# Kernel optimization log

Measured on AMD Instinct MI355X. Metric: run time of the kernel, lower is better.

## Reference

```python
import jax, jax.numpy as jnp
import numpy as np

BS, TLEN, NNODE, DIM = 32, 6, 4, 1500
HID = 128; D2 = 2 * HID
LSTMH, LSTMO, KCONV = 64, 128, 3
CONV_OUT = 191
DECAY = 0.7
WIN, STRIDES = (2, 2), (1, 2)
FEAT_IN = LSTMO * CONV_OUT  # 24448


def _bn(x, p, axis):
    # eval-mode BatchNorm: p = [gamma, beta, running_mean, running_var] stacked [4, C]
    sh = [1] * x.ndim; sh[axis] = -1
    g, b, m, v = (p[i].reshape(sh) for i in range(4))
    return (x - m) * (g * jax.lax.rsqrt(v + 1e-5)) + b


def _conv1d(x, w, pad):  # x [B,C,L], w [O,I,K]
    return jax.lax.conv_general_dilated(x, w, (1,), [(pad, pad)],
                                        dimension_numbers=('NCH', 'OIH', 'NCH'))


def _maxpool2(x):  # MaxPool1d(kernel=2, stride=2, padding=1) with -inf padding
    x = jnp.pad(x, ((0, 0), (0, 0), (1, 1)), constant_values=-jnp.inf)
    return jax.lax.reduce_window(x, -jnp.inf, jax.lax.max, (1, 1, 2), (1, 1, 2), 'VALID')


def _mpnn_block(x, w, s, gw, gb, bnA, tw, tb, bnM):
    # x: [bs, tlen, ns, d]; Conv_GraphST windowing + dot-graph + masked adj + 1-hop MPNN + mean pool
    bs, tlen, ns, d = x.shape
    nw = (tlen - w) // s + 1
    con = jnp.stack([x[:, j * s:j * s + w] for j in range(nw)], axis=1)  # [bs,nw,w,ns,d]
    Xc = con.reshape(bs * nw, w * ns, d)  # node index = t*ns + sensor (time-major)
    f = Xc @ gw + gb
    N = w * ns
    eye = jnp.eye(N, dtype=x.dtype)
    Adj = jnp.einsum('bnd,bmd->bnm', f, f)
    Adj = jax.nn.softmax(jax.nn.leaky_relu(Adj - eye * 1e8), axis=-1) + eye
    t = jnp.arange(N) // ns
    mask = DECAY ** jnp.abs(t[:, None] - t[None, :]).astype(x.dtype)  # Mask_Matrix decay
    Adj = Adj * mask
    Xb = _bn(Xc, bnA, -1)  # BN over feature channel (transpose-BN-transpose in torch)
    h = jnp.einsum('bnm,bmd->bnd', Adj, Xb) @ tw + tb
    h = jax.nn.leaky_relu(_bn(h, bnM, -1))
    return h.reshape(bs, nw, w, ns, -1).mean(axis=2)  # mean pool over window-time


def _pos_encoding(tlen, d):
    pos = jnp.arange(tlen, dtype=jnp.float32)[:, None]
    div = jnp.exp(jnp.arange(0, d, 2, dtype=jnp.float32) * (-np.log(100.0) / d))
    pe = jnp.zeros((tlen, d), jnp.float32)
    return pe.at[:, 0::2].set(jnp.sin(pos * div)).at[:, 1::2].set(jnp.cos(pos * div))


def reference(X, conv1_w, bn1, conv2_w, bn2, conv3_w, bn3,
              map2_w, map2_b, bn_map2,
              g1_w, g1_b, bnA1, th1_w, th1_b, bnM1,
              g2_w, g2_b, bnA2, th2_w, th2_b, bnM2,
              fc1_w, fc1_b, fc2_w, fc2_b, fc3_w, fc3_b, fc4_w, fc4_b):
    X = X.reshape(BS, TLEN, NNODE, -1)
    B = BS * TLEN * NNODE
    a = jnp.transpose(X.reshape(B, -1, 1), (0, 2, 1))  # [B,1,L]
    a = _maxpool2(jax.nn.relu(_bn(_conv1d(a, conv1_w, KCONV // 2), bn1, 1)))
    a = _maxpool2(jax.nn.relu(_bn(_conv1d(a, conv2_w, 2), bn2, 1)))
    a = _maxpool2(jax.nn.relu(_bn(_conv1d(a, conv3_w, 3), bn3, 1)))  # [B,LSTMO,CONV_OUT]
    a = a.reshape(B, -1)
    a = _bn(a @ map2_w + map2_b, bn_map2, -1)
    a = a.reshape(BS, TLEN, NNODE, D2)
    a = a + _pos_encoding(TLEN, D2)[None, :, None, :]  # PE over time, per (batch, node)
    out1 = _mpnn_block(a, WIN[0], STRIDES[0], g1_w, g1_b, bnA1, th1_w, th1_b, bnM1)  # [32,5,4,128]
    out2 = _mpnn_block(a, WIN[1], STRIDES[1], g2_w, g2_b, bnA2, th2_w, th2_b, bnM2)  # [32,3,4,128]
    feats = jnp.concatenate([out1.reshape(BS, -1), out2.reshape(BS, -1)], axis=-1)  # [32,4096]
    h = jax.nn.relu(feats @ fc1_w + fc1_b)
    h = jax.nn.relu(h @ fc2_w + fc2_b)
    h = jax.nn.relu(h @ fc3_w + fc3_b)
    return h @ fc4_w + fc4_b


def setup_inputs():
    key = jax.random.key(0)
    ks = iter(jax.random.split(key, 80))
    def rn(shape, scale=1.0):
        return scale * jax.random.normal(next(ks), shape, jnp.float32)
    def bn(c):
        return jnp.stack([1.0 + 0.1 * rn((c,)), 0.1 * rn((c,)), 0.1 * rn((c,)),
                          1.0 + 0.5 * jax.random.uniform(next(ks), (c,), jnp.float32)])
    def lin(i, o):
        return rn((i, o), 1.0 / np.sqrt(i))
    return {
        'X': rn((BS, TLEN, NNODE, DIM)),
        'conv1_w': rn((LSTMH, 1, KCONV), 0.3),
        'bn1': bn(LSTMH),
        'conv2_w': rn((2 * LSTMH, LSTMH, KCONV), 1.0 / np.sqrt(LSTMH * KCONV)),
        'bn2': bn(2 * LSTMH),
        'conv3_w': rn((LSTMO, 2 * LSTMH, KCONV), 1.0 / np.sqrt(2 * LSTMH * KCONV)),
        'bn3': bn(LSTMO),
        'map2_w': lin(FEAT_IN, D2), 'map2_b': rn((D2,), 0.01), 'bn_map2': bn(D2),
        'g1_w': lin(D2, D2), 'g1_b': rn((D2,), 0.01), 'bnA1': bn(D2),
        'th1_w': lin(D2, HID), 'th1_b': rn((HID,), 0.01), 'bnM1': bn(HID),
        'g2_w': lin(D2, D2), 'g2_b': rn((D2,), 0.01), 'bnA2': bn(D2),
        'th2_w': lin(D2, HID), 'th2_b': rn((HID,), 0.01), 'bnM2': bn(HID),
        'fc1_w': lin(4096, D2), 'fc1_b': rn((D2,), 0.01),
        'fc2_w': lin(D2, D2), 'fc2_b': rn((D2,), 0.01),
        'fc3_w': lin(D2, HID), 'fc3_b': rn((HID,), 0.01),
        'fc4_w': lin(HID, 5), 'fc4_b': rn((5,), 0.01),
    }
```

## Files before the change

### kernel.cpp

```cpp
#include <hip/hip_runtime.h>
#include <hip/hip_bf16.h>

#define L1X   1500
#define L1P   751
#define C1    64
#define L2P   377
#define C2    128
#define L3P   191
#define C3    128
#define FEATK 24448
#define D2    256
#define HIDN  128
#define KSTEPS 764
#define CHUNK 192

typedef __attribute__((ext_vector_type(8))) short bf16x8;
typedef __attribute__((ext_vector_type(4))) float f32x4;

__device__ __forceinline__ short f2bf(float x) {
    union { float f; unsigned u; } v; v.f = x;
    unsigned r = (v.u + 0x7FFFu + ((v.u >> 16) & 1u)) >> 16;
    return (short)r;
}
__device__ __forceinline__ float bf2f(short s) {
    union { float f; unsigned u; } v; v.u = ((unsigned)(unsigned short)s) << 16;
    return v.f;
}

template<int IC, int KB>
__global__ __launch_bounds__(256)
void k_wprep(const float* __restrict__ w, short* __restrict__ WtHi,
             short* __restrict__ WtLo)
{
    int idx = blockIdx.x * 256 + threadIdx.x;
    if (idx >= 3 * KB * 4 * 128 * 8) return;
    int i    = idx & 7;
    int rest = idx >> 3;
    int c    = rest & 127; rest >>= 7;
    int sub  = rest & 3;   rest >>= 2;
    int kb   = rest % KB;
    int tap  = rest / KB;
    int ic   = kb * 32 + sub * 8 + i;
    float x  = w[(c * IC + ic) * 3 + tap];
    short h  = f2bf(x);
    WtHi[idx] = h;
    WtLo[idx] = f2bf(x - bf2f(h));
}

__global__ __launch_bounds__(256)
void k_wmprep(const float* __restrict__ W, short* __restrict__ Wmhi,
              short* __restrict__ Wmlo)
{
    const int ks  = blockIdx.x >> 2;
    const int sub = blockIdx.x & 3;
    const int n   = threadIdx.x;
    const int kbase = ks * 32 + sub * 8;
    bf16x8 vh, vl;
    #pragma unroll
    for (int i = 0; i < 8; ++i) {
        int k = kbase + i;
        int c = k & 127, ip = k >> 7;
        float x = W[(size_t)(c * 191 + ip) * D2 + n];
        short h = f2bf(x);
        vh[i] = h;
        vl[i] = f2bf(x - bf2f(h));
    }
    size_t off = ((size_t)(ks * 4 + sub) * 256 + n) * 8;
    *(bf16x8*)(Wmhi + off) = vh;
    *(bf16x8*)(Wmlo + off) = vl;
}

__global__ __launch_bounds__(256)
void k_zero(float* __restrict__ p, int n)
{
    int i = blockIdx.x * 256 + threadIdx.x;
    if (i < n) p[i] = 0.f;
}

template<int IC, int KB, int CONVLEN, int POOLLEN, bool HL>
__device__ __forceinline__
void conv_mfma_core(const short* __restrict__ WtHi, const short* __restrict__ WtLo,
                    const short* lhi, const short* llo,
                    const float* sc, const float* bc,
                    float* __restrict__ outp, short* __restrict__ ohi,
                    short* __restrict__ olo, int P0)
{
    const int lane = threadIdx.x & 63;
    const int wave = threadIdx.x >> 6;
    const int l15  = lane & 15;
    const int sub  = lane >> 4;

    f32x4 acc[2][8];
    #pragma unroll
    for (int mf = 0; mf < 2; ++mf)
        #pragma unroll
        for (int nf = 0; nf < 8; ++nf)
            acc[mf][nf] = (f32x4){0.f, 0.f, 0.f, 0.f};

    #pragma unroll
    for (int tap = 0; tap < 3; ++tap) {
        #pragma unroll
        for (int kb = 0; kb < KB; ++kb) {
            bf16x8 ah[2], al[2];
            #pragma unroll
            for (int mf = 0; mf < 2; ++mf) {
                int r = wave * 32 + mf * 16 + l15 + tap;
                int chunk = (kb * 4 + sub) ^ (r & 7);
                int off = r * IC + chunk * 8;
                ah[mf] = *(const bf16x8*)(lhi + off);
                al[mf] = *(const bf16x8*)(llo + off);
            }
            const short* wbh = WtHi + (size_t)(((tap * KB + kb) * 4 + sub) * 128) * 8;
            const short* wbl = WtLo + (size_t)(((tap * KB + kb) * 4 + sub) * 128) * 8;
            #pragma unroll
            for (int nf = 0; nf < 8; ++nf) {
                bf16x8 bh = *(const bf16x8*)(wbh + (nf * 16 + l15) * 8);
                bf16x8 bl = *(const bf16x8*)(wbl + (nf * 16 + l15) * 8);
                #pragma unroll
                for (int mf = 0; mf < 2; ++mf) {
                    acc[mf][nf] = __builtin_amdgcn_mfma_f32_16x16x32_bf16(ah[mf], bh, acc[mf][nf], 0, 0, 0);
                    acc[mf][nf] = __builtin_amdgcn_mfma_f32_16x16x32_bf16(ah[mf], bl, acc[mf][nf], 0, 0, 0);
                    acc[mf][nf] = __builtin_amdgcn_mfma_f32_16x16x32_bf16(al[mf], bh, acc[mf][nf], 0, 0, 0);
                }
            }
        }
    }

    #pragma unroll
    for (int mf = 0; mf < 2; ++mf) {
        int mbase = wave * 32 + mf * 16 + sub * 4;
        #pragma unroll
        for (int nf = 0; nf < 8; ++nf) {
            int c = nf * 16 + l15;
            float s = sc[c], bb = bc[c];
            float v[4];
            #pragma unroll
            for (int rg = 0; rg < 4; ++rg) {
                int p = P0 + mbase + rg;
                float x = fmaxf(acc[mf][nf][rg] * s + bb, 0.f);
                v[rg] = (p >= 0 && p < CONVLEN) ? x : 0.f;
            }
            int i0 = (P0 + mbase + 1) >> 1;
            float u0 = fmaxf(v[0], v[1]);
            float u1 = fmaxf(v[2], v[3]);
            if constexpr (HL) {
                if (i0 < POOLLEN) {
                    short h = f2bf(u0);
                    ohi[(size_t)i0 * 128 + c] = h;
                    olo[(size_t)i0 * 128 + c] = f2bf(u0 - bf2f(h));
                }
                if (i0 + 1 < POOLLEN) {
                    short h = f2bf(u1);
                    ohi[(size_t)(i0 + 1) * 128 + c] = h;
                    olo[(size_t)(i0 + 1) * 128 + c] = f2bf(u1 - bf2f(h));
                }
            } else {
                if (i0 < POOLLEN)     outp[(size_t)i0 * 128 + c] = u0;
                if (i0 + 1 < POOLLEN) outp[(size_t)(i0 + 1) * 128 + c] = u1;
            }
        }
    }
}

__global__ __launch_bounds__(256)
void k_conv2_mfma(const float* __restrict__ X, const float* __restrict__ w1,
                  const float* __restrict__ bn1,
                  const short* __restrict__ Wt2hi, const short* __restrict__ Wt2lo,
                  const float* __restrict__ bn2, short* __restrict__ p2hi,
                  short* __restrict__ p2lo, int b_off)
{
    const int blk = blockIdx.x;
    const int bl  = blk / 6, t = blk % 6;
    const int b   = b_off + bl;
    const int P0  = 128 * t - 1;
    const int T0  = 128 * t - 3;
    const int X0  = 256 * t - 8;

    __shared__ __align__(16) float xw[264];
    __shared__ __align__(16) short t1h[130 * 64];
    __shared__ __align__(16) short t1l[130 * 64];
    __shared__ float sb1s[64], sb1b[64], sc2[128], bc2[128];

    const int tid = threadIdx.x;
    for (int g = tid; g < 262; g += 256) {
        int xi = X0 + g;
        xw[g] = (xi >= 0 && xi < L1X) ? X[(size_t)b * L1X + xi] : 0.f;
    }
    if (tid < 64) {
        float s = bn1[tid] * rsqrtf(bn1[192 + tid] + 1e-5f);
        sb1s[tid] = s;
        sb1b[tid] = bn1[64 + tid] - bn1[128 + tid] * s;
    }
    if (tid < 128) {
        float s = bn2[tid] * rsqrtf(bn2[384 + tid] + 1e-5f);
        sc2[tid] = s;
        bc2[tid] = bn2[128 + tid] - bn2[256 + tid] * s;
    }
    __syncthreads();

    for (int idx = tid; idx < 130 * 64; idx += 256) {
        int r = idx >> 6, c = idx & 63;
        int tt = T0 + r;
        float val = 0.f;
        if (tt >= 0 && tt <= 750) {
            float wk0 = w1[c * 3], wk1 = w1[c * 3 + 1], wk2 = w1[c * 3 + 2];
            float s = sb1s[c], bias = sb1b[c];
            float v0 = 0.f, v1 = 0.f;
            int li = 2 * r;
            if (tt >= 1)
                v0 = fmaxf((wk0 * xw[li] + wk1 * xw[li + 1] + wk2 * xw[li + 2]) * s + bias, 0.f);
            if (tt <= 749)
                v1 = fmaxf((wk0 * xw[li + 1] + wk1 * xw[li + 2] + wk2 * xw[li + 3]) * s + bias, 0.f);
            val = fmaxf(v0, v1);
        }
        short h = f2bf(val);
        int chunk = (c >> 3) ^ (r & 7);
        int off = r * 64 + chunk * 8 + (c & 7);
        t1h[off] = h;
        t1l[off] = f2bf(val - bf2f(h));
    }
    __syncthreads();

    conv_mfma_core<64, 2, 753, 377, true>(Wt2hi, Wt2lo, t1h, t1l, sc2, bc2,
                                          nullptr,
                                          p2hi + (size_t)bl * L2P * 128,
                                          p2lo + (size_t)bl * L2P * 128, P0);
}

__global__ __launch_bounds__(256)
void k_conv3_mfma(const short* __restrict__ p2hi, const short* __restrict__ p2lo,
                  const short* __restrict__ Wt3hi, const short* __restrict__ Wt3lo,
                  const float* __restrict__ bn3, short* __restrict__ p3hi,
                  short* __restrict__ p3lo, int b_off)
{
    const int blk = blockIdx.x;
    const int bl  = blk / 3, t = blk % 3;
    const int b   = b_off + bl;
    const int P0  = 128 * t - 1;
    const int I0  = 128 * t - 4;

    __shared__ __align__(16) short t2h[130 * 128];
    __shared__ __align__(16) short t2l[130 * 128];
    __shared__ float sc3[128], bc3[128];

    const int tid = threadIdx.x;
    if (tid < 128) {
        float s = bn3[tid] * rsqrtf(bn3[384 + tid] + 1e-5f);
        sc3[tid] = s;
        bc3[tid] = bn3[128 + tid] - bn3[256 + tid] * s;
    }

    const short* s2h = p2hi + (size_t)bl * L2P * 128;
    const short* s2l = p2lo + (size_t)bl * L2P * 128;
    for (int idx = tid; idx < 130 * 32; idx += 256) {
        int r = idx >> 5, q = idx & 31;
        int pr = I0 + r;
        short4 vh = make_short4(0, 0, 0, 0), vl = make_short4(0, 0, 0, 0);
        if (pr >= 0 && pr < L2P) {
            vh = *(const short4*)(s2h + (size_t)pr * 128 + q * 4);
            vl = *(const short4*)(s2l + (size_t)pr * 128 + q * 4);
        }
        int chunk = (q >> 1) ^ (r & 7);
        int off = r * 128 + chunk * 8 + (q & 1) * 4;
        *(short4*)(t2h + off) = vh;
        *(short4*)(t2l + off) = vl;
    }
    __syncthreads();

    conv_mfma_core<128, 4, 381, 191, true>(Wt3hi, Wt3lo, t2h, t2l, sc3, bc3,
                                           nullptr,
                                           p3hi + (size_t)b * FEATK,
                                           p3lo + (size_t)b * FEATK, P0);
}

__global__ __launch_bounds__(256)
void k_map2_mfma(const short* __restrict__ Ahi, const short* __restrict__ Alo,
                 const short* __restrict__ Wmhi, const short* __restrict__ Wmlo,
                 float* __restrict__ accum)
{
    const int kt   = blockIdx.x % 48;
    const int mt   = blockIdx.x / 48;
    const int tid  = threadIdx.x;
    const int lane = tid & 63, wave = tid >> 6;
    const int l15  = lane & 15, sub = lane >> 4;
    const int wm   = wave >> 1, wn = wave & 1;
    const int m0   = mt * 64;

    const int s0 = kt * 16;
    const int s1 = (s0 + 16 < KSTEPS) ? s0 + 16 : KSTEPS;

    __shared__ __align__(16) short Ah[2][64 * 40];
    __shared__ __align__(16) short Al[2][64 * 40];

    const int r  = tid >> 2;
    const int kb = tid & 3;
    const size_t abase = (size_t)(m0 + r) * FEATK + kb * 8;
    const int    lbase = r * 40 + kb * 8;

    f32x4 acc[2][8];
    #pragma unroll
    for (int mf = 0; mf < 2; ++mf)
        #pragma unroll
        for (int nf = 0; nf < 8; ++nf)
            acc[mf][nf] = (f32x4){0.f, 0.f, 0.f, 0.f};

    *(bf16x8*)&Ah[0][lbase] = *(const bf16x8*)(Ahi + abase + (size_t)s0 * 32);
    *(bf16x8*)&Al[0][lbase] = *(const bf16x8*)(Alo + abase + (size_t)s0 * 32);

    int cur = 0;
    for (int s = s0; s < s1; ++s) {
        __syncthreads();
        if (s + 1 < s1) {
            *(bf16x8*)&Ah[cur ^ 1][lbase] = *(const bf16x8*)(Ahi + abase + (size_t)(s + 1) * 32);
            *(bf16x8*)&Al[cur ^ 1][lbase] = *(const bf16x8*)(Alo + abase + (size_t)(s + 1) * 32);
        }
        bf16x8 ah[2], al[2];
        #pragma unroll
        for (int mf = 0; mf < 2; ++mf) {
            int off = (wm * 32 + mf * 16 + l15) * 40 + sub * 8;
            ah[mf] = *(const bf16x8*)&Ah[cur][off];
            al[mf] = *(const bf16x8*)&Al[cur][off];
        }
        const short* wb = Wmhi + ((size_t)(s * 4 + sub) * 256 + wn * 128) * 8;
        const short* wl = Wmlo + ((size_t)(s * 4 + sub) * 256 + wn * 128) * 8;
        #pragma unroll
        for (int nf = 0; nf < 8; ++nf) {
            bf16x8 bh = *(const bf16x8*)(wb + (nf * 16 + l15) * 8);
            bf16x8 bl = *(const bf16x8*)(wl + (nf * 16 + l15) * 8);
            #pragma unroll
            for (int mf = 0; mf < 2; ++mf) {
                acc[mf][nf] = __builtin_amdgcn_mfma_f32_16x16x32_bf16(ah[mf], bh, acc[mf][nf], 0, 0, 0);
                acc[mf][nf] = __builtin_amdgcn_mfma_f32_16x16x32_bf16(ah[mf], bl, acc[mf][nf], 0, 0, 0);
                acc[mf][nf] = __builtin_amdgcn_mfma_f32_16x16x32_bf16(al[mf], bh, acc[mf][nf], 0, 0, 0);
            }
        }
        cur ^= 1;
    }

    float* acct = accum + (size_t)(kt & 7) * 196608;
    #pragma unroll
    for (int mf = 0; mf < 2; ++mf) {
        int mrow = m0 + wm * 32 + mf * 16 + sub * 4;
        #pragma unroll
        for (int nf = 0; nf < 8; ++nf) {
            int n = wn * 128 + nf * 16 + l15;
            #pragma unroll
            for (int rg = 0; rg < 4; ++rg)
                atomicAdd(&acct[(size_t)(mrow + rg) * D2 + n], acc[mf][nf][rg]);
        }
    }
}

__global__ __launch_bounds__(256)
void k_map2fin(const float* __restrict__ accum, const float* __restrict__ mb,
               const float* __restrict__ bn, float* __restrict__ out)
{
    const int row = blockIdx.x;
    const int n   = threadIdx.x;
    float acc = 0.f;
    #pragma unroll
    for (int c = 0; c < 8; ++c)
        acc += accum[(size_t)c * 196608 + (size_t)row * D2 + n];

    float s    = bn[n] * rsqrtf(bn[768 + n] + 1e-5f);
    float beta = bn[256 + n];
    float mu   = bn[512 + n];
    float bias = mb[n];
    int   jj   = n >> 1;
    float freq = expf((float)(2 * jj) * (-4.605170185988092f / 256.f));
    int   t    = (row >> 2) % 6;
    float ang  = (float)t * freq;
    float pe   = (n & 1) ? cosf(ang) : sinf(ang);
    out[(size_t)row * D2 + n] = (acc + bias - mu) * s + beta + pe;
}

__global__ __launch_bounds__(256)
void k_mpnn(const float* __restrict__ a_pe, const float* __restrict__ gw,
            const float* __restrict__ gb, const float* __restrict__ bnA,
            const float* __restrict__ tw, const float* __restrict__ tb_,
            const float* __restrict__ bnM, float* __restrict__ feats,
            int nw, int stride, int base)
{
    const int g  = blockIdx.x;
    const int b  = g / nw, wi = g % nw;
    const int tid = threadIdx.x;

    __shared__ float Xc[8][256];
    __shared__ float Xb[8][256];
    __shared__ float Fs[8][256];
    __shared__ float Adj[8][8];
    __shared__ float hsm[8][128];

    for (int e = tid; e < 2048; e += 256) {
        int nn = e >> 8, d = e & 255;
        int tt = nn >> 2, sn = nn & 3;
        float v = a_pe[(((size_t)(b * 6) + (wi * stride + tt)) * 4 + sn) * D2 + d];
        Xc[nn][d] = v;
        float s = bnA[d] * rsqrtf(bnA[768 + d] + 1e-5f);
        Xb[nn][d] = (v - bnA[512 + d]) * s + bnA[256 + d];
    }
    __syncthreads();

    {
        const int d = tid;
        #pragma unroll
        for (int nn = 0; nn < 8; ++nn) {
            float acc = gb[d];
            for (int k = 0; k < 256; ++k) acc += Xc[nn][k] * gw[(size_t)k * D2 + d];
            Fs[nn][d] = acc;
        }
    }
    __syncthreads();

    if (tid < 64) {
        int nn = tid >> 3, m = tid & 7;
        float s = 0.f;
        for (int d = 0; d < 256; ++d) s += Fs[nn][d] * Fs[m][d];
        if (nn == m) s -= 1e8f;
        s = (s > 0.f) ? s : 0.01f * s;
        Adj[nn][m] = s;
    }
    __syncthreads();

    if (tid < 8) {
        int nn = tid;
        float mx = -1e30f;
        for (int m = 0; m < 8; ++m) mx = fmaxf(mx, Adj[nn][m]);
        float ex[8]; float sum = 0.f;
        for (int m = 0; m < 8; ++m) { ex[m] = expf(Adj[nn][m] - mx); sum += ex[m]; }
        float inv = 1.f / sum;
        for (int m = 0; m < 8; ++m) {
            float v = ex[m] * inv + ((nn == m) ? 1.f : 0.f);
            v *= ((nn >> 2) == (m >> 2)) ? 1.f : 0.7f;
            Adj[nn][m] = v;
        }
    }
    __syncthreads();

    {
        const int d = tid;
        float hm[8];
        #pragma unroll
        for (int nn = 0; nn < 8; ++nn) {
            float a = 0.f;
            #pragma unroll
            for (int m = 0; m < 8; ++m) a += Adj[nn][m] * Xb[m][d];
            hm[nn] = a;
        }
        #pragma unroll
        for (int nn = 0; nn < 8; ++nn) Fs[nn][d] = hm[nn];
    }
    __syncthreads();

    {
        const int o = tid & 127, half = tid >> 7;
        float ms  = bnM[o] * rsqrtf(bnM[384 + o] + 1e-5f);
        float mbe = bnM[128 + o], mmu = bnM[256 + o];
        #pragma unroll
        for (int q = 0; q < 4; ++q) {
            int nn = half + 2 * q;
            float acc = tb_[o];
            for (int d = 0; d < 256; ++d) acc += Fs[nn][d] * tw[(size_t)d * HIDN + o];
            float y = (acc - mmu) * ms + mbe;
            hsm[nn][o] = (y > 0.f) ? y : 0.01f * y;
        }
    }
    __syncthreads();

    for (int e = tid; e < 512; e += 256) {
        int sn = e >> 7, o = e & 127;
        feats[(size_t)b * 4096 + base + (wi * 4 + sn) * HIDN + o] =
            0.5f * (hsm[sn][o] + hsm[4 + sn][o]);
    }
}

__global__ __launch_bounds__(256)
void k_fc1(const float* __restrict__ feats, const float* __restrict__ w1f,
           float* __restrict__ partfc)
{
    const int kc = blockIdx.x >> 3;
    const int nc = blockIdx.x & 7;
    const int tid = threadIdx.x;

    __shared__ float fst[32 * 257];

    for (int idx = tid; idx < 32 * 256; idx += 256) {
        int r = idx >> 8, k = idx & 255;
        fst[r * 257 + k] = feats[(size_t)r * 4096 + kc * 256 + k];
    }
    __syncthreads();

    const int c  = tid & 31;
    const int rg = tid >> 5;
    const float* wp = w1f + (size_t)(kc * 256) * 256 + nc * 32 + c;

    float acc[4] = {0.f, 0.f, 0.f, 0.f};
    for (int k = 0; k < 256; ++k) {
        float wv = wp[(size_t)k * 256];
        #pragma unroll
        for (int j = 0; j < 4; ++j)
            acc[j] += fst[(rg * 4 + j) * 257 + k] * wv;
    }
    #pragma unroll
    for (int j = 0; j < 4; ++j)
        partfc[((size_t)kc * 32 + rg * 4 + j) * 256 + nc * 32 + c] = acc[j];
}

__global__ __launch_bounds__(256)
void k_fc_rest(const float* __restrict__ partfc,
               const float* __restrict__ b1f,
               const float* __restrict__ w2f, const float* __restrict__ b2f,
               const float* __restrict__ w3f, const float* __restrict__ b3f,
               const float* __restrict__ w4f, const float* __restrict__ b4f,
               float* __restrict__ out)
{
    const int b = blockIdx.x;
    const int n = threadIdx.x;
    __shared__ float h1[256], h2[256], h3[128];

    {
        float acc = b1f[n];
        #pragma unroll
        for (int kc = 0; kc < 16; ++kc)
            acc += partfc[((size_t)kc * 32 + b) * 256 + n];
        h1[n] = fmaxf(acc, 0.f);
    }
    __syncthreads();
    {
        float acc = b2f[n];
        for (int k = 0; k < 256; ++k) acc += h1[k] * w2f[(size_t)k * 256 + n];
        h2[n] = fmaxf(acc, 0.f);
    }
    __syncthreads();
    if (n < 128) {
        float acc = b3f[n];
        for (int k = 0; k < 256; ++k) acc += h2[k] * w3f[(size_t)k * 128 + n];
        h3[n] = fmaxf(acc, 0.f);
    }
    __syncthreads();
    if (n < 5) {
        float acc = b4f[n];
        for (int k = 0; k < 128; ++k) acc += h3[k] * w4f[(size_t)k * 5 + n];
        out[b * 5 + n] = acc;
    }
}

extern "C" void kernel_launch(void* const* d_in, const int* in_sizes, int n_in,
                              void* d_out, int out_size, void* d_ws, size_t ws_size,
                              hipStream_t stream)
{
    const float* X      = (const float*)d_in[0];
    const float* w1     = (const float*)d_in[1];
    const float* bn1    = (const float*)d_in[2];
    const float* w2     = (const float*)d_in[3];
    const float* bn2    = (const float*)d_in[4];
    const float* w3     = (const float*)d_in[5];
    const float* bn3    = (const float*)d_in[6];
    const float* map2w  = (const float*)d_in[7];
    const float* map2b  = (const float*)d_in[8];
    const float* bnm2   = (const float*)d_in[9];
    const float* g1w    = (const float*)d_in[10];
    const float* g1b    = (const float*)d_in[11];
    const float* bnA1   = (const float*)d_in[12];
    const float* th1w   = (const float*)d_in[13];
    const float* th1b   = (const float*)d_in[14];
    const float* bnM1   = (const float*)d_in[15];
    const float* g2w    = (const float*)d_in[16];
    const float* g2b    = (const float*)d_in[17];
    const float* bnA2   = (const float*)d_in[18];
    const float* th2w   = (const float*)d_in[19];
    const float* th2b   = (const float*)d_in[20];
    const float* bnM2   = (const float*)d_in[21];
    const float* fc1w   = (const float*)d_in[22];
    const float* fc1b   = (const float*)d_in[23];
    const float* fc2w   = (const float*)d_in[24];
    const float* fc2b   = (const float*)d_in[25];
    const float* fc3w   = (const float*)d_in[26];
    const float* fc3b   = (const float*)d_in[27];
    const float* fc4w   = (const float*)d_in[28];
    const float* fc4b   = (const float*)d_in[29];
    float* out = (float*)d_out;

    float* ws = (float*)d_ws;
    const size_t SZ_P2 = (size_t)CHUNK * L2P * 128;
    short* p2hi  = (short*)ws;
    short* p2lo  = p2hi + SZ_P2;
    short* Wmhi  = (short*)ws;
    short* Wmlo  = Wmhi + 6258688;
    float* accum = (float*)(Wmlo + 6258688);
    float* after  = ws + 9264384;
    short* p3hi   = (short*)after;
    short* p3lo   = p3hi + 18776064;
    float* a_pe   = (float*)(p3lo + 18776064);
    float* feats  = a_pe + 196608;
    short* Wt2hi  = (short*)(feats + 131072);
    short* Wt2lo  = Wt2hi + 24576;
    short* Wt3hi  = Wt2lo + 24576;
    short* Wt3lo  = Wt3hi + 49152;
    float* partfc = (float*)(Wt3lo + 49152);

    k_wprep<64, 2><<<96, 256, 0, stream>>>(w2, Wt2hi, Wt2lo);
    k_wprep<128, 4><<<192, 256, 0, stream>>>(w3, Wt3hi, Wt3lo);

    for (int boff = 0; boff < 768; boff += CHUNK) {
        k_conv2_mfma<<<CHUNK * 6, 256, 0, stream>>>(X, w1, bn1, Wt2hi, Wt2lo, bn2,
                                                    p2hi, p2lo, boff);
        k_conv3_mfma<<<CHUNK * 3, 256, 0, stream>>>(p2hi, p2lo, Wt3hi, Wt3lo, bn3,
                                                    p3hi, p3lo, boff);
    }
    k_wmprep<<<KSTEPS * 4, 256, 0, stream>>>(map2w, Wmhi, Wmlo);
    k_zero<<<(8 * 196608 + 255) / 256, 256, 0, stream>>>(accum, 8 * 196608);
    k_map2_mfma<<<576, 256, 0, stream>>>(p3hi, p3lo, Wmhi, Wmlo, accum);
    k_map2fin<<<768, 256, 0, stream>>>(accum, map2b, bnm2, a_pe);
    k_mpnn<<<160, 256, 0, stream>>>(a_pe, g1w, g1b, bnA1, th1w, th1b, bnM1,
                                    feats, 5, 1, 0);
    k_mpnn<<<96, 256, 0, stream>>>(a_pe, g2w, g2b, bnA2, th2w, th2b, bnM2,
                                   feats, 3, 2, 2560);
    k_fc1<<<128, 256, 0, stream>>>(feats, fc1w, partfc);
    k_fc_rest<<<32, 256, 0, stream>>>(partfc, fc1b, fc2w, fc2b, fc3w, fc3b,
                                      fc4w, fc4b, out);
}
```

Baseline: 679.0 us.

## Halve conv3 LDS by staging hi and lo activations sequentially; vectorize conv1 fill

conv3 now keeps a single shared tile instead of separate hi and lo tiles. It first runs the hi activation pass against the hi and lo weights, then reloads the lo activations into the same buffer and runs lo times hi-weight MFMAs. The LDS footprint roughly halves, which could let more blocks fit per CU, at the cost of an extra barrier and a second global load phase. conv1 now computes four channels per thread with float4 weight loads and short4 LDS stores, and the two mpnn launches are merged into one grid to save a launch.

```diff
diff --git a/kernel.cpp b/kernel.cpp
--- a/kernel.cpp
+++ b/kernel.cpp
@@ -77,13 +77,12 @@
     if (i < n) p[i] = 0.f;
 }
 
-template<int IC, int KB, int CONVLEN, int POOLLEN, bool HL>
+template<int IC, int KB, int CONVLEN, int POOLLEN>
 __device__ __forceinline__
 void conv_mfma_core(const short* __restrict__ WtHi, const short* __restrict__ WtLo,
                     const short* lhi, const short* llo,
                     const float* sc, const float* bc,
-                    float* __restrict__ outp, short* __restrict__ ohi,
-                    short* __restrict__ olo, int P0)
+                    short* __restrict__ ohi, short* __restrict__ olo, int P0)
 {
     const int lane = threadIdx.x & 63;
     const int wave = threadIdx.x >> 6;
@@ -143,20 +142,15 @@
             int i0 = (P0 + mbase + 1) >> 1;
             float u0 = fmaxf(v[0], v[1]);
             float u1 = fmaxf(v[2], v[3]);
-            if constexpr (HL) {
-                if (i0 < POOLLEN) {
-                    short h = f2bf(u0);
-                    ohi[(size_t)i0 * 128 + c] = h;
-                    olo[(size_t)i0 * 128 + c] = f2bf(u0 - bf2f(h));
-                }
-                if (i0 + 1 < POOLLEN) {
-                    short h = f2bf(u1);
-                    ohi[(size_t)(i0 + 1) * 128 + c] = h;
-                    olo[(size_t)(i0 + 1) * 128 + c] = f2bf(u1 - bf2f(h));
-                }
-            } else {
-                if (i0 < POOLLEN)     outp[(size_t)i0 * 128 + c] = u0;
-                if (i0 + 1 < POOLLEN) outp[(size_t)(i0 + 1) * 128 + c] = u1;
+            if (i0 < POOLLEN) {
+                short h = f2bf(u0);
+                ohi[(size_t)i0 * 128 + c] = h;
+                olo[(size_t)i0 * 128 + c] = f2bf(u0 - bf2f(h));
+            }
+            if (i0 + 1 < POOLLEN) {
+                short h = f2bf(u1);
+                ohi[(size_t)(i0 + 1) * 128 + c] = h;
+                olo[(size_t)(i0 + 1) * 128 + c] = f2bf(u1 - bf2f(h));
             }
         }
     }
@@ -198,33 +192,44 @@
     }
     __syncthreads();
 
-    for (int idx = tid; idx < 130 * 64; idx += 256) {
-        int r = idx >> 6, c = idx & 63;
+    for (int q2 = tid; q2 < 130 * 16; q2 += 256) {
+        int r  = q2 >> 4;
+        int cq = (q2 & 15) * 4;
         int tt = T0 + r;
-        float val = 0.f;
+        short4 sh = make_short4(0, 0, 0, 0), sl = make_short4(0, 0, 0, 0);
         if (tt >= 0 && tt <= 750) {
-            float wk0 = w1[c * 3], wk1 = w1[c * 3 + 1], wk2 = w1[c * 3 + 2];
-            float s = sb1s[c], bias = sb1b[c];
-            float v0 = 0.f, v1 = 0.f;
             int li = 2 * r;
-            if (tt >= 1)
-                v0 = fmaxf((wk0 * xw[li] + wk1 * xw[li + 1] + wk2 * xw[li + 2]) * s + bias, 0.f);
-            if (tt <= 749)
-                v1 = fmaxf((wk0 * xw[li + 1] + wk1 * xw[li + 2] + wk2 * xw[li + 3]) * s + bias, 0.f);
-            val = fmaxf(v0, v1);
-        }
-        short h = f2bf(val);
-        int chunk = (c >> 3) ^ (r & 7);
-        int off = r * 64 + chunk * 8 + (c & 7);
-        t1h[off] = h;
-        t1l[off] = f2bf(val - bf2f(h));
-    }
-    __syncthreads();
-
-    conv_mfma_core<64, 2, 753, 377, true>(Wt2hi, Wt2lo, t1h, t1l, sc2, bc2,
-                                          nullptr,
-                                          p2hi + (size_t)bl * L2P * 128,
-                                          p2lo + (size_t)bl * L2P * 128, P0);
+            float xa = xw[li], xb = xw[li + 1], xc = xw[li + 2], xd = xw[li + 3];
+            float4 wA = *(const float4*)(w1 + cq * 3);
+            float4 wB = *(const float4*)(w1 + cq * 3 + 4);
+            float4 wC = *(const float4*)(w1 + cq * 3 + 8);
+            float wv[4][3] = {{wA.x, wA.y, wA.z}, {wA.w, wB.x, wB.y},
+                              {wB.z, wB.w, wC.x}, {wC.y, wC.z, wC.w}};
+            #pragma unroll
+            for (int j = 0; j < 4; ++j) {
+                int c = cq + j;
+                float s = sb1s[c], bias = sb1b[c];
+                float v0 = 0.f, v1 = 0.f;
+                if (tt >= 1)
+                    v0 = fmaxf((wv[j][0] * xa + wv[j][1] * xb + wv[j][2] * xc) * s + bias, 0.f);
+                if (tt <= 749)
+                    v1 = fmaxf((wv[j][0] * xb + wv[j][1] * xc + wv[j][2] * xd) * s + bias, 0.f);
+                float val = fmaxf(v0, v1);
+                short h = f2bf(val);
+                ((short*)&sh)[j] = h;
+                ((short*)&sl)[j] = f2bf(val - bf2f(h));
+            }
+        }
+        int chunk = (cq >> 3) ^ (r & 7);
+        int off = r * 64 + chunk * 8 + (cq & 7);
+        *(short4*)(t1h + off) = sh;
+        *(short4*)(t1l + off) = sl;
+    }
+    __syncthreads();
+
+    conv_mfma_core<64, 2, 753, 377>(Wt2hi, Wt2lo, t1h, t1l, sc2, bc2,
+                                    p2hi + (size_t)bl * L2P * 128,
+                                    p2lo + (size_t)bl * L2P * 128, P0);
 }
 
 __global__ __launch_bounds__(256)
@@ -239,11 +244,13 @@
     const int P0  = 128 * t - 1;
     const int I0  = 128 * t - 4;
 
-    __shared__ __align__(16) short t2h[130 * 128];
-    __shared__ __align__(16) short t2l[130 * 128];
+    __shared__ __align__(16) short t2s[130 * 128];
     __shared__ float sc3[128], bc3[128];
 
-    const int tid = threadIdx.x;
+    const int tid  = threadIdx.x;
+    const int lane = tid & 63, wave = tid >> 6;
+    const int l15  = lane & 15, sub = lane >> 4;
+
     if (tid < 128) {
         float s = bn3[tid] * rsqrtf(bn3[384 + tid] + 1e-5f);
         sc3[tid] = s;
@@ -252,25 +259,114 @@
 
     const short* s2h = p2hi + (size_t)bl * L2P * 128;
     const short* s2l = p2lo + (size_t)bl * L2P * 128;
+
     for (int idx = tid; idx < 130 * 32; idx += 256) {
         int r = idx >> 5, q = idx & 31;
         int pr = I0 + r;
-        short4 vh = make_short4(0, 0, 0, 0), vl = make_short4(0, 0, 0, 0);
-        if (pr >= 0 && pr < L2P) {
-            vh = *(const short4*)(s2h + (size_t)pr * 128 + q * 4);
-            vl = *(const short4*)(s2l + (size_t)pr * 128 + q * 4);
-        }
+        short4 vh = make_short4(0, 0, 0, 0);
+        if (pr >= 0 && pr < L2P) vh = *(const short4*)(s2h + (size_t)pr * 128 + q * 4);
         int chunk = (q >> 1) ^ (r & 7);
-        int off = r * 128 + chunk * 8 + (q & 1) * 4;
-        *(short4*)(t2h + off) = vh;
-        *(short4*)(t2l + off) = vl;
-    }
-    __syncthreads();
-
-    conv_mfma_core<128, 4, 381, 191, true>(Wt3hi, Wt3lo, t2h, t2l, sc3, bc3,
-                                           nullptr,
-                                           p3hi + (size_t)b * FEATK,
-                                           p3lo + (size_t)b * FEATK, P0);
+        *(short4*)(t2s + r * 128 + chunk * 8 + (q & 1) * 4) = vh;
+    }
+    __syncthreads();
+
+    f32x4 acc[2][8];
+    #pragma unroll
+    for (int mf = 0; mf < 2; ++mf)
+        #pragma unroll
+        for (int nf = 0; nf < 8; ++nf)
+            acc[mf][nf] = (f32x4){0.f, 0.f, 0.f, 0.f};
+
+    #pragma unroll
+    for (int tap = 0; tap < 3; ++tap) {
+        #pragma unroll
+        for (int kb = 0; kb < 4; ++kb) {
+            bf16x8 ah[2];
+            #pragma unroll
+            for (int mf = 0; mf < 2; ++mf) {
+                int r = wave * 32 + mf * 16 + l15 + tap;
+                int chunk = (kb * 4 + sub) ^ (r & 7);
+                ah[mf] = *(const bf16x8*)(t2s + r * 128 + chunk * 8);
+            }
+            const short* wbh = Wt3hi + (size_t)(((tap * 4 + kb) * 4 + sub) * 128) * 8;
+            const short* wbl = Wt3lo + (size_t)(((tap * 4 + kb) * 4 + sub) * 128) * 8;
+            #pragma unroll
+            for (int nf = 0; nf < 8; ++nf) {
+                bf16x8 bh = *(const bf16x8*)(wbh + (nf * 16 + l15) * 8);
+                bf16x8 bl = *(const bf16x8*)(wbl + (nf * 16 + l15) * 8);
+                #pragma unroll
+                for (int mf = 0; mf < 2; ++mf) {
+                    acc[mf][nf] = __builtin_amdgcn_mfma_f32_16x16x32_bf16(ah[mf], bh, acc[mf][nf], 0, 0, 0);
+                    acc[mf][nf] = __builtin_amdgcn_mfma_f32_16x16x32_bf16(ah[mf], bl, acc[mf][nf], 0, 0, 0);
+                }
+            }
+        }
+    }
+
+    __syncthreads();
+    for (int idx = tid; idx < 130 * 32; idx += 256) {
+        int r = idx >> 5, q = idx & 31;
+        int pr = I0 + r;
+        short4 vl = make_short4(0, 0, 0, 0);
+        if (pr >= 0 && pr < L2P) vl = *(const short4*)(s2l + (size_t)pr * 128 + q * 4);
+        int chunk = (q >> 1) ^ (r & 7);
+        *(short4*)(t2s + r * 128 + chunk * 8 + (q & 1) * 4) = vl;
+    }
+    __syncthreads();
+
+    #pragma unroll
+    for (int tap = 0; tap < 3; ++tap) {
+        #pragma unroll
+        for (int kb = 0; kb < 4; ++kb) {
+            bf16x8 al[2];
+            #pragma unroll
+            for (int mf = 0; mf < 2; ++mf) {
+                int r = wave * 32 + mf * 16 + l15 + tap;
+                int chunk = (kb * 4 + sub) ^ (r & 7);
+                al[mf] = *(const bf16x8*)(t2s + r * 128 + chunk * 8);
+            }
+            const short* wbh = Wt3hi + (size_t)(((tap * 4 + kb) * 4 + sub) * 128) * 8;
+            #pragma unroll
+            for (int nf = 0; nf < 8; ++nf) {
+                bf16x8 bh = *(const bf16x8*)(wbh + (nf * 16 + l15) * 8);
+                #pragma unroll
+                for (int mf = 0; mf < 2; ++mf)
+                    acc[mf][nf] = __builtin_amdgcn_mfma_f32_16x16x32_bf16(al[mf], bh, acc[mf][nf], 0, 0, 0);
+            }
+        }
+    }
+
+    short* ohi = p3hi + (size_t)b * FEATK;
+    short* olo = p3lo + (size_t)b * FEATK;
+    #pragma unroll
+    for (int mf = 0; mf < 2; ++mf) {
+        int mbase = wave * 32 + mf * 16 + sub * 4;
+        #pragma unroll
+        for (int nf = 0; nf < 8; ++nf) {
+            int c = nf * 16 + l15;
+            float s = sc3[c], bb = bc3[c];
+            float v[4];
+            #pragma unroll
+            for (int rg = 0; rg < 4; ++rg) {
+                int p = P0 + mbase + rg;
+                float x = fmaxf(acc[mf][nf][rg] * s + bb, 0.f);
+                v[rg] = (p >= 0 && p < 381) ? x : 0.f;
+            }
+            int i0 = (P0 + mbase + 1) >> 1;
+            float u0 = fmaxf(v[0], v[1]);
+            float u1 = fmaxf(v[2], v[3]);
+            if (i0 < L3P) {
+                short h = f2bf(u0);
+                ohi[(size_t)i0 * 128 + c] = h;
+                olo[(size_t)i0 * 128 + c] = f2bf(u0 - bf2f(h));
+            }
+            if (i0 + 1 < L3P) {
+                short h = f2bf(u1);
+                ohi[(size_t)(i0 + 1) * 128 + c] = h;
+                olo[(size_t)(i0 + 1) * 128 + c] = f2bf(u1 - bf2f(h));
+            }
+        }
+    }
 }
 
 __global__ __launch_bounds__(256)
@@ -375,13 +471,27 @@
 }
 
 __global__ __launch_bounds__(256)
-void k_mpnn(const float* __restrict__ a_pe, const float* __restrict__ gw,
-            const float* __restrict__ gb, const float* __restrict__ bnA,
-            const float* __restrict__ tw, const float* __restrict__ tb_,
-            const float* __restrict__ bnM, float* __restrict__ feats,
-            int nw, int stride, int base)
-{
-    const int g  = blockIdx.x;
+void k_mpnn_all(const float* __restrict__ a_pe,
+                const float* __restrict__ g1w, const float* __restrict__ g1b,
+                const float* __restrict__ bnA1, const float* __restrict__ th1w,
+                const float* __restrict__ th1b, const float* __restrict__ bnM1,
+                const float* __restrict__ g2w, const float* __restrict__ g2b,
+                const float* __restrict__ bnA2, const float* __restrict__ th2w,
+                const float* __restrict__ th2b, const float* __restrict__ bnM2,
+                float* __restrict__ feats)
+{
+    const bool second = blockIdx.x >= 160;
+    const int g    = second ? blockIdx.x - 160 : blockIdx.x;
+    const int nw   = second ? 3 : 5;
+    const int stride = second ? 2 : 1;
+    const int base = second ? 2560 : 0;
+    const float* gw  = second ? g2w : g1w;
+    const float* gb  = second ? g2b : g1b;
+    const float* bnA = second ? bnA2 : bnA1;
+    const float* tw  = second ? th2w : th1w;
+    const float* tb_ = second ? th2b : th1b;
+    const float* bnM = second ? bnM2 : bnM1;
+
     const int b  = g / nw, wi = g % nw;
     const int tid = threadIdx.x;
 
@@ -612,10 +722,8 @@
     k_zero<<<(8 * 196608 + 255) / 256, 256, 0, stream>>>(accum, 8 * 196608);
     k_map2_mfma<<<576, 256, 0, stream>>>(p3hi, p3lo, Wmhi, Wmlo, accum);
     k_map2fin<<<768, 256, 0, stream>>>(accum, map2b, bnm2, a_pe);
-    k_mpnn<<<160, 256, 0, stream>>>(a_pe, g1w, g1b, bnA1, th1w, th1b, bnM1,
-                                    feats, 5, 1, 0);
-    k_mpnn<<<96, 256, 0, stream>>>(a_pe, g2w, g2b, bnA2, th2w, th2b, bnM2,
-                                   feats, 3, 2, 2560);
+    k_mpnn_all<<<256, 256, 0, stream>>>(a_pe, g1w, g1b, bnA1, th1w, th1b, bnM1,
+                                        g2w, g2b, bnA2, th2w, th2b, bnM2, feats);
     k_fc1<<<128, 256, 0, stream>>>(feats, fc1w, partfc);
     k_fc_rest<<<32, 256, 0, stream>>>(partfc, fc1b, fc2w, fc2b, fc3w, fc3b,
                                       fc4w, fc4b, out);
```

Result: slower. 706.2 us (+4.0%).
